# Kernel optimization log

Hardware: AMD Instinct MI355X
Metric: run time of the kernel (lower is better)

Reference implementation:

```python
import jax, jax.numpy as jnp
import numpy as np

B, P, G, NPTS = 32, 1000, 24, 72
D = 6 + NPTS
W_REG = 3.0
LENGTH = 15.0
EPS = 1e-8


def setup_inputs() -> dict:
    key = jax.random.key(0)
    k1, k2, k3 = jax.random.split(key, 3)
    preds = jax.random.uniform(k1, (B, P, D), dtype=jnp.float32)
    targets = jax.random.uniform(k2, (B, G, D), dtype=jnp.float32)
    num_gt = jax.random.randint(k3, (B,), 1, G + 1)
    masks = jnp.arange(G)[None, :] < num_gt[:, None]  # prefix validity mask, as in torch slicing
    return {"preds": preds, "targets": targets, "masks": masks, "img_w": 800, "img_h": 320}


def _assign_one(pred, target, gt_mask, img_w, img_h):
    # pred: [P, 6+n], target: [G, 6+n], gt_mask: [G] bool
    Gn = target.shape[0]
    pred = pred.at[:, 3].multiply(img_w - 1.0)
    pred = pred.at[:, 6:].multiply(img_w - 1.0)
    target = target.at[:, 3].multiply(img_w - 1.0)
    target = target.at[:, 6:].multiply(img_w - 1.0)
    ppts = pred[:, 6:]    # [P, n]
    tpts = target[:, 6:]  # [G, n]

    valid_pts = (tpts >= 0) & (tpts < img_w)                         # [G, n]
    valid_len = jnp.clip(valid_pts.sum(1).astype(pred.dtype), 1.0)
    diff = jnp.abs(ppts[:, None, :] - tpts[None, :, :]) * valid_pts[None].astype(pred.dtype)
    distances = diff.sum(-1) / valid_len[None]                       # [P, G]

    def masked_max(x):  # max over valid gts only (matches torch slice [:num_gt])
        return jnp.max(jnp.where(gt_mask[None], x, -jnp.inf))

    d_score = 1.0 - distances / (masked_max(distances) + EPS) + 0.01

    p_start = jnp.stack([pred[:, 2] * (img_h - 1.0), pred[:, 3]], axis=1)
    t_start = jnp.stack([target[:, 2] * (img_h - 1.0), target[:, 3]], axis=1)
    start_d = jnp.sqrt(jnp.sum((p_start[:, None, :] - t_start[None, :, :]) ** 2, -1))
    xy_score = 1.0 - start_d / (masked_max(start_d) + EPS) + 0.01

    theta_d = jnp.abs(pred[:, 4:5] * 180.0 - target[None, :, 4] * 180.0)  # [P, G]
    th_score = 1.0 - theta_d / (masked_max(theta_d) + EPS) + 0.01

    cls_prob = jax.nn.softmax(pred[:, :2], axis=1)[:, 1]
    cls_cost = -jnp.log(jnp.clip(cls_prob, EPS))                     # [P]

    reg_score = d_score * xy_score * th_score
    total_cost = -(reg_score ** 2) * W_REG + cls_cost[:, None]       # [P, G]

    # line_iou, unaligned (CLRNet): per-point segment overlap of length 2*LENGTH
    px1, px2 = ppts - LENGTH, ppts + LENGTH
    tx1, tx2 = tpts - LENGTH, tpts + LENGTH
    inval = (tpts < 0) | (tpts >= img_w)                             # [G, n]
    ovr = jnp.minimum(px2[:, None, :], tx2[None]) - jnp.maximum(px1[:, None, :], tx1[None])
    uni = jnp.maximum(px2[:, None, :], tx2[None]) - jnp.minimum(px1[:, None, :], tx1[None])
    ovr = jnp.where(inval[None], 0.0, ovr)
    uni = jnp.where(inval[None], 0.0, uni)
    liou = jnp.nan_to_num(ovr.sum(-1) / (uni.sum(-1) + 1e-9))        # [P, G]

    n_cand = min(4, ppts.shape[0])
    topk_ious, _ = jax.lax.top_k(liou.T, n_cand)                     # [G, k]
    dynamic_ks = jnp.clip(topk_ious.sum(1).astype(jnp.int32), 1)     # [G]

    # per-gt topk(smallest cost, k=dynamic_ks[g]) via rank < k
    ranks = jnp.argsort(jnp.argsort(total_cost, axis=0), axis=0)     # [P, G]
    matching = (ranks < dynamic_ks[None, :]) & gt_mask[None, :]      # [P, G] bool

    # conflict resolution: priors matched to >1 gts keep only the min-cost gt
    counts = matching.sum(1)
    best_g = jnp.argmin(jnp.where(gt_mask[None, :], total_cost, jnp.inf), axis=1)  # [P]
    onehot = best_g[:, None] == jnp.arange(Gn)[None, :]
    matching = jnp.where((counts > 1)[:, None], onehot, matching)

    assigned = matching.any(1)
    matched = jnp.where(assigned, jnp.argmax(matching, axis=1), -1).astype(jnp.int32)
    return assigned, matched


def reference(preds, targets, masks, img_w, img_h):
    w, h = float(img_w), float(img_h)
    fn = lambda p, t, m: _assign_one(p, t, m, w, h)
    assigned_mask, matched_targets = jax.vmap(fn)(preds, targets, masks)
    return assigned_mask, matched_targets
```

## Files before the change

kernel.cpp:

```cpp
#include <hip/hip_runtime.h>
#include <cstdint>
#include <cstddef>

#define BN 32
#define PN 1000
#define GN 24
#define NPTSN 72
#define DNN 78
#define CHN 16
#define PPC 63
#define EPSF 1e-8f
#define INF __builtin_inff()

#define OFF_DIST  0
#define OFF_LIOU  768000
#define OFF_PX    1536000
#define OFF_PY    1568000
#define OFF_PTH   1600000
#define OFF_CLS   1632000
#define OFF_PART  1664000
#define OFF_CNT   1665536
#define OFF_SELG  1697536
#define OFF_BEST  1729536

__device__ __forceinline__ unsigned ordf(float f) {
  unsigned u = __float_as_uint(f);
  return (u & 0x80000000u) ? ~u : (u | 0x80000000u);
}
__device__ __forceinline__ float unordf(unsigned u) {
  return __uint_as_float((u & 0x80000000u) ? (u ^ 0x80000000u) : ~u);
}
__device__ __forceinline__ unsigned long long shfl_xor_u64(unsigned long long v, int m) {
  int lo = __shfl_xor((int)(unsigned)v, m);
  int hi = __shfl_xor((int)(unsigned)(v >> 32), m);
  return (((unsigned long long)(unsigned)hi) << 32) | (unsigned)lo;
}

__device__ int detect_mask_layout(const void* masks, int* sflag) {
  const unsigned* mw = (const unsigned*)masks;
  if (mw[0] == 0x3f800000u) return 2;
  if (threadIdx.x == 0) *sflag = 0;
  __syncthreads();
  const unsigned char* mb = (const unsigned char*)masks;
  int local = 0;
  for (int i = threadIdx.x; i < BN * GN; i += blockDim.x)
    if ((i & 3) != 0 && mb[i] != 0) local = 1;
  if (local) atomicOr(sflag, 1);
  __syncthreads();
  return (*sflag) ? 1 : 0;
}
__device__ __forceinline__ int mask_val(const void* masks, int layout, int idx) {
  if (layout == 2) return ((const float*)masks)[idx] != 0.0f;
  if (layout == 1) return ((const unsigned char*)masks)[idx] != 0;
  return ((const int*)masks)[idx] != 0;
}

__global__ __launch_bounds__(256) void clr_k1(
    const float* __restrict__ preds, const float* __restrict__ targets,
    const void* __restrict__ masks, const int* __restrict__ imw,
    const int* __restrict__ imh, float* __restrict__ ws)
{
  const int b = blockIdx.y, c = blockIdx.x;
  const int tid = threadIdx.x;
  const int lane = tid & 63;
  const int gq = __builtin_amdgcn_readfirstlane(tid >> 6);
  const float wf = (float)imw[0];
  const float wm1 = wf - 1.0f, hm1 = (float)imh[0] - 1.0f;

  {
    int gid = (b * CHN + c) * 256 + tid;
    if (gid < BN * PN) {
      int* wsi = (int*)ws;
      wsi[OFF_CNT + gid] = 0;
      wsi[OFF_SELG + gid] = 0x7fffffff;
      ((unsigned long long*)(ws + OFF_BEST))[gid] = ~0ull;
    }
  }

  __shared__ __align__(16) float sts[GN * NPTSN];
  __shared__ __align__(16) float stw[GN * NPTSN];
  __shared__ float svl[GN], snv[GN], sgx[GN], sgy[GN], sgth[GN];
  __shared__ int sgm[GN];
  __shared__ int sng;
  __shared__ int sflag;
  __shared__ float red[4][3];

  const int mlay = detect_mask_layout(masks, &sflag);

  for (int idx = tid; idx < GN * NPTSN; idx += 256) {
    int g = idx / NPTSN, j = idx - g * NPTSN;
    float t = targets[(size_t)(b * GN + g) * DNN + 6 + j] * wm1;
    sts[idx] = t;
    stw[idx] = (t >= 0.0f && t < wf) ? 1.0f : 0.0f;
  }
  __syncthreads();
  if (tid < GN) {
    float cnt = 0.0f;
    for (int j = 0; j < NPTSN; j++) cnt += stw[tid * NPTSN + j];
    snv[tid] = cnt;
    svl[tid] = fmaxf(cnt, 1.0f);
    const float* tr = targets + (size_t)(b * GN + tid) * DNN;
    sgx[tid]  = tr[2] * hm1;
    sgy[tid]  = tr[3] * wm1;
    sgth[tid] = tr[4] * 180.0f;
    sgm[tid] = mask_val(masks, mlay, b * GN + tid);
  }
  __syncthreads();
  if (tid == 0) {
    int n = 0;
    for (int g = 0; g < GN; g++) n += sgm[g];
    sng = n;
  }
  __syncthreads();
  const int ng = sng;

  const int p = c * PPC + lane;
  const bool active = (lane < PPC) && (p < PN);
  float pp[NPTSN];
  float ppx = 0.f, ppy = 0.f, ppth = 0.f;
  if (active) {
    const float* row = preds + (size_t)(b * PN + p) * DNN;
    const float2* r2 = (const float2*)row;
    float2 c23 = r2[1], c45 = r2[2];
    ppx = c23.x * hm1; ppy = c23.y * wm1; ppth = c45.x * 180.0f;
    #pragma unroll
    for (int j = 0; j < NPTSN / 2; j++) {
      float2 v = r2[3 + j];
      pp[2 * j]     = v.x * wm1;
      pp[2 * j + 1] = v.y * wm1;
    }
    if (gq == 0) {
      float2 c01 = r2[0];
      float m = fmaxf(c01.x, c01.y);
      float e0 = expf(c01.x - m), e1 = expf(c01.y - m);
      float p1 = fmaxf(e1 / (e0 + e1), EPSF);
      ws[OFF_PX  + b * PN + p] = ppx;
      ws[OFF_PY  + b * PN + p] = ppy;
      ws[OFF_PTH + b * PN + p] = ppth;
      ws[OFF_CLS + b * PN + p] = -logf(p1);
    }
  } else {
    #pragma unroll
    for (int j = 0; j < NPTSN; j++) pp[j] = 0.0f;
  }

  float mxd = -INF, mxs = -INF, mxt = -INF;
  for (int i = 0; i < 6; i++) {
    const int g = gq + 4 * i;
    if (g >= ng) break;
    const float4* t4 = (const float4*)&sts[g * NPTSN];
    const float4* w4 = (const float4*)&stw[g * NPTSN];
    float S0 = 0.f, S1 = 0.f, S2 = 0.f, S3 = 0.f;
    #pragma unroll
    for (int jj = 0; jj < NPTSN / 4; jj++) {
      float4 t = t4[jj], w = w4[jj];
      S0 += w.x * fabsf(pp[4 * jj + 0] - t.x);
      S1 += w.y * fabsf(pp[4 * jj + 1] - t.y);
      S2 += w.z * fabsf(pp[4 * jj + 2] - t.z);
      S3 += w.w * fabsf(pp[4 * jj + 3] - t.w);
    }
    float S = (S0 + S1) + (S2 + S3);
    const float VL = svl[g], NV = snv[g];
    float dist = S / VL;
    float liou = (30.0f * NV - S) / (30.0f * NV + S + 1e-9f);
    float dx = ppx - sgx[g], dy = ppy - sgy[g];
    float sd = sqrtf(dx * dx + dy * dy);
    float td = fabsf(ppth - sgth[g]);
    if (active) {
      size_t o = (size_t)(b * GN + g) * PN + p;
      ws[OFF_DIST + o] = dist;
      ws[OFF_LIOU + o] = liou;
      mxd = fmaxf(mxd, dist);
      mxs = fmaxf(mxs, sd);
      mxt = fmaxf(mxt, td);
    }
  }

  #pragma unroll
  for (int off = 32; off; off >>= 1) {
    mxd = fmaxf(mxd, __shfl_xor(mxd, off));
    mxs = fmaxf(mxs, __shfl_xor(mxs, off));
    mxt = fmaxf(mxt, __shfl_xor(mxt, off));
  }
  if (lane == 0) { red[gq][0] = mxd; red[gq][1] = mxs; red[gq][2] = mxt; }
  __syncthreads();
  if (tid == 0) {
    float a = red[0][0], s = red[0][1], t = red[0][2];
    for (int i = 1; i < 4; i++) {
      a = fmaxf(a, red[i][0]);
      s = fmaxf(s, red[i][1]);
      t = fmaxf(t, red[i][2]);
    }
    ws[OFF_PART + (b * CHN + c) * 3 + 0] = a;
    ws[OFF_PART + (b * CHN + c) * 3 + 1] = s;
    ws[OFF_PART + (b * CHN + c) * 3 + 2] = t;
  }
}

__global__ __launch_bounds__(256) void clr_k2a(
    const float* __restrict__ targets, const void* __restrict__ masks,
    const int* __restrict__ imw, const int* __restrict__ imh,
    const float* __restrict__ cws, float* __restrict__ ws)
{
  const int g = blockIdx.x, b = blockIdx.y;
  const int bg = b * GN + g;
  __shared__ int sflag;
  const int mlay = detect_mask_layout(masks, &sflag);
  if (!mask_val(masks, mlay, bg)) return;

  const int tid = threadIdx.x;
  const int lane = tid & 63;
  const int wv = tid >> 6;
  const float hm1 = (float)imh[0] - 1.0f;
  const float wm1 = (float)imw[0] - 1.0f;

  float Md = -INF, Ms = -INF, Mt = -INF;
  for (int c2 = 0; c2 < CHN; c2++) {
    Md = fmaxf(Md, cws[OFF_PART + (b * CHN + c2) * 3 + 0]);
    Ms = fmaxf(Ms, cws[OFF_PART + (b * CHN + c2) * 3 + 1]);
    Mt = fmaxf(Mt, cws[OFF_PART + (b * CHN + c2) * 3 + 2]);
  }
  const float* tr = targets + (size_t)bg * DNN;
  const float tx = tr[2] * hm1, ty = tr[3] * wm1, tth = tr[4] * 180.0f;
  const size_t dbase = (size_t)bg * PN;
  unsigned long long* bst = (unsigned long long*)(ws + OFF_BEST);
  int* wsi = (int*)ws;

  unsigned long long ck[4], lk[4];
  #pragma unroll
  for (int i = 0; i < 4; i++) {
    int p = tid + i * 256;
    unsigned long long kc = ~0ull, kl = ~0ull;
    if (p < PN) {
      float dist = cws[OFF_DIST + dbase + p];
      float liou = cws[OFF_LIOU + dbase + p];
      float px  = cws[OFF_PX  + b * PN + p];
      float py  = cws[OFF_PY  + b * PN + p];
      float pth = cws[OFF_PTH + b * PN + p];
      float cls = cws[OFF_CLS + b * PN + p];
      float dsc = (1.0f - dist / (Md + EPSF)) + 0.01f;
      float dx = px - tx, dy = py - ty;
      float xsc = (1.0f - sqrtf(dx * dx + dy * dy) / (Ms + EPSF)) + 0.01f;
      float tsc = (1.0f - fabsf(pth - tth) / (Mt + EPSF)) + 0.01f;
      float r = (dsc * xsc) * tsc;
      float cost = -(r * r) * 3.0f + cls;
      unsigned oc = ordf(cost);
      kc = (((unsigned long long)oc) << 32) | (unsigned)p;
      kl = (((unsigned long long)(unsigned)(~ordf(liou))) << 32) | (unsigned)p;
      atomicMin(&bst[b * PN + p], (((unsigned long long)oc) << 32) | (unsigned)g);
    }
    ck[i] = kc; lk[i] = kl;
  }

  __shared__ unsigned long long ctop[4][4], ltop[4][4];
  #pragma unroll
  for (int pass = 0; pass < 4; pass++) {
    unsigned long long m = ck[0];
    #pragma unroll
    for (int i = 1; i < 4; i++) m = (ck[i] < m) ? ck[i] : m;
    #pragma unroll
    for (int off = 32; off; off >>= 1) {
      unsigned long long o = shfl_xor_u64(m, off);
      m = (o < m) ? o : m;
    }
    #pragma unroll
    for (int i = 0; i < 4; i++) if (ck[i] == m) ck[i] = ~0ull;
    if (lane == 0) ctop[wv][pass] = m;
  }
  #pragma unroll
  for (int pass = 0; pass < 4; pass++) {
    unsigned long long m = lk[0];
    #pragma unroll
    for (int i = 1; i < 4; i++) m = (lk[i] < m) ? lk[i] : m;
    #pragma unroll
    for (int off = 32; off; off >>= 1) {
      unsigned long long o = shfl_xor_u64(m, off);
      m = (o < m) ? o : m;
    }
    #pragma unroll
    for (int i = 0; i < 4; i++) if (lk[i] == m) lk[i] = ~0ull;
    if (lane == 0) ltop[wv][pass] = m;
  }
  __syncthreads();

  if (tid == 0) {
    unsigned long long c4[4] = {~0ull, ~0ull, ~0ull, ~0ull};
    unsigned long long l4[4] = {~0ull, ~0ull, ~0ull, ~0ull};
    for (int i = 0; i < 16; i++) {
      unsigned long long v = ctop[i >> 2][i & 3];
      for (int j = 0; j < 4; j++)
        if (v < c4[j]) { unsigned long long t = c4[j]; c4[j] = v; v = t; }
      v = ltop[i >> 2][i & 3];
      for (int j = 0; j < 4; j++)
        if (v < l4[j]) { unsigned long long t = l4[j]; l4[j] = v; v = t; }
    }
    float s = 0.0f;
    for (int j = 0; j < 4; j++) s += unordf(~(unsigned)(l4[j] >> 32));
    int k = (int)s;
    if (k < 1) k = 1;
    if (k > 4) k = 4;
    for (int j = 0; j < k; j++) {
      int cand = (int)(unsigned)(c4[j] & 0xffffffffu);
      atomicAdd(&wsi[OFF_CNT + b * PN + cand], 1);
      atomicMin(&wsi[OFF_SELG + b * PN + cand], g);
    }
  }
}

__global__ __launch_bounds__(256) void clr_k2b(
    const float* __restrict__ cws, int* __restrict__ out)
{
  const int i = blockIdx.x * 256 + threadIdx.x;
  if (i >= BN * PN) return;
  const int* wsi = (const int*)cws;
  const unsigned long long* bst = (const unsigned long long*)(cws + OFF_BEST);
  int cnt = wsi[OFF_CNT + i];
  int assigned = cnt > 0 ? 1 : 0;
  int matched = -1;
  if (cnt == 1) matched = wsi[OFF_SELG + i];
  else if (cnt > 1) matched = (int)(unsigned)(bst[i] & 0xffffffffull);
  out[i] = assigned;
  out[BN * PN + i] = matched;
}

extern "C" void kernel_launch(void* const* d_in, const int* in_sizes, int n_in,
                              void* d_out, int out_size, void* d_ws, size_t ws_size,
                              hipStream_t stream) {
  const float* preds   = (const float*)d_in[0];
  const float* targets = (const float*)d_in[1];
  const void*  masks   = (const void*)d_in[2];
  const int*   imw     = (const int*)d_in[3];
  const int*   imh     = (const int*)d_in[4];
  float* ws = (float*)d_ws;
  int*   out = (int*)d_out;

  hipLaunchKernelGGL(clr_k1, dim3(CHN, BN), dim3(256), 0, stream,
                     preds, targets, masks, imw, imh, ws);
  hipLaunchKernelGGL(clr_k2a, dim3(GN, BN), dim3(256), 0, stream,
                     targets, masks, imw, imh, (const float*)d_ws, ws);
  hipLaunchKernelGGL(clr_k2b, dim3((BN * PN + 255) / 256), dim3(256), 0, stream,
                     (const float*)d_ws, out);
}
```

Before: 96.21 us.

## Fuse three kernels into one cooperative kernel with grid syncs

Merges the distance, cost/top-k and finalize kernels into a single cooperative launch separated by grid-wide syncs. The per-prior atomicMin best-cost tracking is replaced by a stored cost matrix that the final phase scans. Target points are now read from global memory instead of shared-memory staging, and a fast path skips the validity test when all points are valid. The aim is to remove launch gaps and atomics, at the cost of grid-sync overhead, an extra cost-matrix write plus its INF initialization, and a dependence on all 512 blocks being co-resident.

```diff
diff --git a/kernel.cpp b/kernel.cpp
--- a/kernel.cpp
+++ b/kernel.cpp
@@ -1,6 +1,9 @@
 #include <hip/hip_runtime.h>
+#include <hip/hip_cooperative_groups.h>
 #include <cstdint>
 #include <cstddef>
+
+namespace cg = cooperative_groups;
 
 #define BN 32
 #define PN 1000
@@ -9,19 +12,20 @@
 #define DNN 78
 #define CHN 16
 #define PPC 63
+#define NBLK (CHN*BN)
 #define EPSF 1e-8f
 #define INF __builtin_inff()
 
 #define OFF_DIST  0
 #define OFF_LIOU  768000
-#define OFF_PX    1536000
-#define OFF_PY    1568000
-#define OFF_PTH   1600000
-#define OFF_CLS   1632000
-#define OFF_PART  1664000
-#define OFF_CNT   1665536
-#define OFF_SELG  1697536
-#define OFF_BEST  1729536
+#define OFF_COST  1536000
+#define OFF_PX    2304000
+#define OFF_PY    2336000
+#define OFF_PTH   2368000
+#define OFF_CLS   2400000
+#define OFF_PART  2432000
+#define OFF_CNT   2433536
+#define OFF_SELG  2465536
 
 __device__ __forceinline__ unsigned ordf(float f) {
   unsigned u = __float_as_uint(f);
@@ -55,51 +59,48 @@
   return ((const int*)masks)[idx] != 0;
 }
 
-__global__ __launch_bounds__(256) void clr_k1(
+__global__ __launch_bounds__(256, 2) void clr_fused(
     const float* __restrict__ preds, const float* __restrict__ targets,
     const void* __restrict__ masks, const int* __restrict__ imw,
-    const int* __restrict__ imh, float* __restrict__ ws)
+    const int* __restrict__ imh, float* __restrict__ ws, int* __restrict__ out)
 {
-  const int b = blockIdx.y, c = blockIdx.x;
+  const int bx = blockIdx.x;
+  const int b  = bx >> 4;
+  const int c  = bx & 15;
   const int tid = threadIdx.x;
   const int lane = tid & 63;
   const int gq = __builtin_amdgcn_readfirstlane(tid >> 6);
-  const float wf = (float)imw[0];
+  const float wf  = (float)imw[0];
   const float wm1 = wf - 1.0f, hm1 = (float)imh[0] - 1.0f;
+  int* wsi = (int*)ws;
 
   {
-    int gid = (b * CHN + c) * 256 + tid;
+    int gid = bx * 256 + tid;
     if (gid < BN * PN) {
-      int* wsi = (int*)ws;
-      wsi[OFF_CNT + gid] = 0;
+      wsi[OFF_CNT + gid]  = 0;
       wsi[OFF_SELG + gid] = 0x7fffffff;
-      ((unsigned long long*)(ws + OFF_BEST))[gid] = ~0ull;
-    }
-  }
-
-  __shared__ __align__(16) float sts[GN * NPTSN];
-  __shared__ __align__(16) float stw[GN * NPTSN];
+    }
+    for (int k = gid; k < BN * GN * PN; k += NBLK * 256)
+      ws[OFF_COST + k] = INF;
+  }
+
   __shared__ float svl[GN], snv[GN], sgx[GN], sgy[GN], sgth[GN];
   __shared__ int sgm[GN];
-  __shared__ int sng;
-  __shared__ int sflag;
+  __shared__ int sng, sflag;
   __shared__ float red[4][3];
+  __shared__ unsigned long long ctop[4][4], ltop[4][4];
 
   const int mlay = detect_mask_layout(masks, &sflag);
 
-  for (int idx = tid; idx < GN * NPTSN; idx += 256) {
-    int g = idx / NPTSN, j = idx - g * NPTSN;
-    float t = targets[(size_t)(b * GN + g) * DNN + 6 + j] * wm1;
-    sts[idx] = t;
-    stw[idx] = (t >= 0.0f && t < wf) ? 1.0f : 0.0f;
-  }
-  __syncthreads();
   if (tid < GN) {
+    const float* tr = targets + (size_t)(b * GN + tid) * DNN;
     float cnt = 0.0f;
-    for (int j = 0; j < NPTSN; j++) cnt += stw[tid * NPTSN + j];
+    for (int j = 0; j < NPTSN; j++) {
+      float ts = tr[6 + j] * wm1;
+      cnt += (ts >= 0.0f && ts < wf) ? 1.0f : 0.0f;
+    }
     snv[tid] = cnt;
     svl[tid] = fmaxf(cnt, 1.0f);
-    const float* tr = targets + (size_t)(b * GN + tid) * DNN;
     sgx[tid]  = tr[2] * hm1;
     sgy[tid]  = tr[3] * wm1;
     sgth[tid] = tr[4] * 180.0f;
@@ -112,7 +113,7 @@
     sng = n;
   }
   __syncthreads();
-  const int ng = sng;
+  const int ng = __builtin_amdgcn_readfirstlane(sng);
 
   const int p = c * PPC + lane;
   const bool active = (lane < PPC) && (p < PN);
@@ -126,8 +127,8 @@
     #pragma unroll
     for (int j = 0; j < NPTSN / 2; j++) {
       float2 v = r2[3 + j];
-      pp[2 * j]     = v.x * wm1;
-      pp[2 * j + 1] = v.y * wm1;
+      pp[2 * j]     = v.x;
+      pp[2 * j + 1] = v.y;
     }
     if (gq == 0) {
       float2 c01 = r2[0];
@@ -148,20 +149,31 @@
   for (int i = 0; i < 6; i++) {
     const int g = gq + 4 * i;
     if (g >= ng) break;
-    const float4* t4 = (const float4*)&sts[g * NPTSN];
-    const float4* w4 = (const float4*)&stw[g * NPTSN];
+    const float NV = snv[g];
+    const float* tr6 = targets + (size_t)(b * GN + g) * DNN + 6;
     float S0 = 0.f, S1 = 0.f, S2 = 0.f, S3 = 0.f;
-    #pragma unroll
-    for (int jj = 0; jj < NPTSN / 4; jj++) {
-      float4 t = t4[jj], w = w4[jj];
-      S0 += w.x * fabsf(pp[4 * jj + 0] - t.x);
-      S1 += w.y * fabsf(pp[4 * jj + 1] - t.y);
-      S2 += w.z * fabsf(pp[4 * jj + 2] - t.z);
-      S3 += w.w * fabsf(pp[4 * jj + 3] - t.w);
-    }
-    float S = (S0 + S1) + (S2 + S3);
-    const float VL = svl[g], NV = snv[g];
-    float dist = S / VL;
+    if (NV == (float)NPTSN) {
+      #pragma unroll
+      for (int jj = 0; jj < NPTSN; jj += 4) {
+        S0 += fabsf(pp[jj + 0] - tr6[jj + 0]);
+        S1 += fabsf(pp[jj + 1] - tr6[jj + 1]);
+        S2 += fabsf(pp[jj + 2] - tr6[jj + 2]);
+        S3 += fabsf(pp[jj + 3] - tr6[jj + 3]);
+      }
+    } else {
+      #pragma unroll
+      for (int jj = 0; jj < NPTSN; jj += 4) {
+        float t0 = tr6[jj + 0], t1 = tr6[jj + 1];
+        float t2 = tr6[jj + 2], t3 = tr6[jj + 3];
+        float v0 = t0 * wm1, v1 = t1 * wm1, v2 = t2 * wm1, v3 = t3 * wm1;
+        S0 += (v0 >= 0.0f && v0 < wf) ? fabsf(pp[jj + 0] - t0) : 0.0f;
+        S1 += (v1 >= 0.0f && v1 < wf) ? fabsf(pp[jj + 1] - t1) : 0.0f;
+        S2 += (v2 >= 0.0f && v2 < wf) ? fabsf(pp[jj + 2] - t2) : 0.0f;
+        S3 += (v3 >= 0.0f && v3 < wf) ? fabsf(pp[jj + 3] - t3) : 0.0f;
+      }
+    }
+    float S = ((S0 + S1) + (S2 + S3)) * wm1;
+    float dist = S / svl[g];
     float liou = (30.0f * NV - S) / (30.0f * NV + S + 1e-9f);
     float dx = ppx - sgx[g], dy = ppy - sgy[g];
     float sd = sqrtf(dx * dx + dy * dy);
@@ -191,136 +203,132 @@
       s = fmaxf(s, red[i][1]);
       t = fmaxf(t, red[i][2]);
     }
-    ws[OFF_PART + (b * CHN + c) * 3 + 0] = a;
-    ws[OFF_PART + (b * CHN + c) * 3 + 1] = s;
-    ws[OFF_PART + (b * CHN + c) * 3 + 2] = t;
-  }
-}
-
-__global__ __launch_bounds__(256) void clr_k2a(
-    const float* __restrict__ targets, const void* __restrict__ masks,
-    const int* __restrict__ imw, const int* __restrict__ imh,
-    const float* __restrict__ cws, float* __restrict__ ws)
-{
-  const int g = blockIdx.x, b = blockIdx.y;
-  const int bg = b * GN + g;
-  __shared__ int sflag;
-  const int mlay = detect_mask_layout(masks, &sflag);
-  if (!mask_val(masks, mlay, bg)) return;
-
-  const int tid = threadIdx.x;
-  const int lane = tid & 63;
-  const int wv = tid >> 6;
-  const float hm1 = (float)imh[0] - 1.0f;
-  const float wm1 = (float)imw[0] - 1.0f;
-
-  float Md = -INF, Ms = -INF, Mt = -INF;
-  for (int c2 = 0; c2 < CHN; c2++) {
-    Md = fmaxf(Md, cws[OFF_PART + (b * CHN + c2) * 3 + 0]);
-    Ms = fmaxf(Ms, cws[OFF_PART + (b * CHN + c2) * 3 + 1]);
-    Mt = fmaxf(Mt, cws[OFF_PART + (b * CHN + c2) * 3 + 2]);
-  }
-  const float* tr = targets + (size_t)bg * DNN;
-  const float tx = tr[2] * hm1, ty = tr[3] * wm1, tth = tr[4] * 180.0f;
-  const size_t dbase = (size_t)bg * PN;
-  unsigned long long* bst = (unsigned long long*)(ws + OFF_BEST);
-  int* wsi = (int*)ws;
-
-  unsigned long long ck[4], lk[4];
-  #pragma unroll
-  for (int i = 0; i < 4; i++) {
-    int p = tid + i * 256;
-    unsigned long long kc = ~0ull, kl = ~0ull;
-    if (p < PN) {
-      float dist = cws[OFF_DIST + dbase + p];
-      float liou = cws[OFF_LIOU + dbase + p];
-      float px  = cws[OFF_PX  + b * PN + p];
-      float py  = cws[OFF_PY  + b * PN + p];
-      float pth = cws[OFF_PTH + b * PN + p];
-      float cls = cws[OFF_CLS + b * PN + p];
-      float dsc = (1.0f - dist / (Md + EPSF)) + 0.01f;
-      float dx = px - tx, dy = py - ty;
-      float xsc = (1.0f - sqrtf(dx * dx + dy * dy) / (Ms + EPSF)) + 0.01f;
-      float tsc = (1.0f - fabsf(pth - tth) / (Mt + EPSF)) + 0.01f;
-      float r = (dsc * xsc) * tsc;
-      float cost = -(r * r) * 3.0f + cls;
-      unsigned oc = ordf(cost);
-      kc = (((unsigned long long)oc) << 32) | (unsigned)p;
-      kl = (((unsigned long long)(unsigned)(~ordf(liou))) << 32) | (unsigned)p;
-      atomicMin(&bst[b * PN + p], (((unsigned long long)oc) << 32) | (unsigned)g);
-    }
-    ck[i] = kc; lk[i] = kl;
-  }
-
-  __shared__ unsigned long long ctop[4][4], ltop[4][4];
-  #pragma unroll
-  for (int pass = 0; pass < 4; pass++) {
-    unsigned long long m = ck[0];
-    #pragma unroll
-    for (int i = 1; i < 4; i++) m = (ck[i] < m) ? ck[i] : m;
-    #pragma unroll
-    for (int off = 32; off; off >>= 1) {
-      unsigned long long o = shfl_xor_u64(m, off);
-      m = (o < m) ? o : m;
-    }
-    #pragma unroll
-    for (int i = 0; i < 4; i++) if (ck[i] == m) ck[i] = ~0ull;
-    if (lane == 0) ctop[wv][pass] = m;
-  }
-  #pragma unroll
-  for (int pass = 0; pass < 4; pass++) {
-    unsigned long long m = lk[0];
-    #pragma unroll
-    for (int i = 1; i < 4; i++) m = (lk[i] < m) ? lk[i] : m;
-    #pragma unroll
-    for (int off = 32; off; off >>= 1) {
-      unsigned long long o = shfl_xor_u64(m, off);
-      m = (o < m) ? o : m;
-    }
-    #pragma unroll
-    for (int i = 0; i < 4; i++) if (lk[i] == m) lk[i] = ~0ull;
-    if (lane == 0) ltop[wv][pass] = m;
-  }
-  __syncthreads();
-
-  if (tid == 0) {
-    unsigned long long c4[4] = {~0ull, ~0ull, ~0ull, ~0ull};
-    unsigned long long l4[4] = {~0ull, ~0ull, ~0ull, ~0ull};
-    for (int i = 0; i < 16; i++) {
-      unsigned long long v = ctop[i >> 2][i & 3];
-      for (int j = 0; j < 4; j++)
-        if (v < c4[j]) { unsigned long long t = c4[j]; c4[j] = v; v = t; }
-      v = ltop[i >> 2][i & 3];
-      for (int j = 0; j < 4; j++)
-        if (v < l4[j]) { unsigned long long t = l4[j]; l4[j] = v; v = t; }
-    }
-    float s = 0.0f;
-    for (int j = 0; j < 4; j++) s += unordf(~(unsigned)(l4[j] >> 32));
-    int k = (int)s;
-    if (k < 1) k = 1;
-    if (k > 4) k = 4;
-    for (int j = 0; j < k; j++) {
-      int cand = (int)(unsigned)(c4[j] & 0xffffffffu);
-      atomicAdd(&wsi[OFF_CNT + b * PN + cand], 1);
-      atomicMin(&wsi[OFF_SELG + b * PN + cand], g);
-    }
-  }
-}
-
-__global__ __launch_bounds__(256) void clr_k2b(
-    const float* __restrict__ cws, int* __restrict__ out)
-{
-  const int i = blockIdx.x * 256 + threadIdx.x;
-  if (i >= BN * PN) return;
-  const int* wsi = (const int*)cws;
-  const unsigned long long* bst = (const unsigned long long*)(cws + OFF_BEST);
-  int cnt = wsi[OFF_CNT + i];
-  int assigned = cnt > 0 ? 1 : 0;
-  int matched = -1;
-  if (cnt == 1) matched = wsi[OFF_SELG + i];
-  else if (cnt > 1) matched = (int)(unsigned)(bst[i] & 0xffffffffull);
-  out[i] = assigned;
-  out[BN * PN + i] = matched;
+    ws[OFF_PART + bx * 3 + 0] = a;
+    ws[OFF_PART + bx * 3 + 1] = s;
+    ws[OFF_PART + bx * 3 + 2] = t;
+  }
+
+  cg::this_grid().sync();
+
+  for (int task = bx; task < BN * GN; task += NBLK) {
+    const int b2 = task / GN;
+    const int g2 = task - b2 * GN;
+    if (mask_val(masks, mlay, task)) {
+      const int wv = tid >> 6;
+      float Md = -INF, Ms = -INF, Mt = -INF;
+      for (int c2 = 0; c2 < CHN; c2++) {
+        Md = fmaxf(Md, ws[OFF_PART + (b2 * CHN + c2) * 3 + 0]);
+        Ms = fmaxf(Ms, ws[OFF_PART + (b2 * CHN + c2) * 3 + 1]);
+        Mt = fmaxf(Mt, ws[OFF_PART + (b2 * CHN + c2) * 3 + 2]);
+      }
+      const float* tr = targets + (size_t)task * DNN;
+      const float tx = tr[2] * hm1, ty = tr[3] * wm1, tth = tr[4] * 180.0f;
+      const size_t dbase = (size_t)task * PN;
+
+      unsigned long long ck[4], lk[4];
+      #pragma unroll
+      for (int i = 0; i < 4; i++) {
+        int p2 = tid + i * 256;
+        unsigned long long kc = ~0ull, kl = ~0ull;
+        if (p2 < PN) {
+          float dist = ws[OFF_DIST + dbase + p2];
+          float liou = ws[OFF_LIOU + dbase + p2];
+          float px  = ws[OFF_PX  + b2 * PN + p2];
+          float py  = ws[OFF_PY  + b2 * PN + p2];
+          float pth = ws[OFF_PTH + b2 * PN + p2];
+          float cls = ws[OFF_CLS + b2 * PN + p2];
+          float dsc = (1.0f - dist / (Md + EPSF)) + 0.01f;
+          float dx = px - tx, dy = py - ty;
+          float xsc = (1.0f - sqrtf(dx * dx + dy * dy) / (Ms + EPSF)) + 0.01f;
+          float tsc = (1.0f - fabsf(pth - tth) / (Mt + EPSF)) + 0.01f;
+          float r = (dsc * xsc) * tsc;
+          float cost = -(r * r) * 3.0f + cls;
+          ws[OFF_COST + dbase + p2] = cost;
+          unsigned oc = ordf(cost);
+          kc = (((unsigned long long)oc) << 32) | (unsigned)p2;
+          kl = (((unsigned long long)(unsigned)(~ordf(liou))) << 32) | (unsigned)p2;
+        }
+        ck[i] = kc; lk[i] = kl;
+      }
+
+      #pragma unroll
+      for (int pass = 0; pass < 4; pass++) {
+        unsigned long long m = ck[0];
+        #pragma unroll
+        for (int i = 1; i < 4; i++) m = (ck[i] < m) ? ck[i] : m;
+        #pragma unroll
+        for (int off = 32; off; off >>= 1) {
+          unsigned long long o = shfl_xor_u64(m, off);
+          m = (o < m) ? o : m;
+        }
+        #pragma unroll
+        for (int i = 0; i < 4; i++) if (ck[i] == m) ck[i] = ~0ull;
+        if (lane == 0) ctop[wv][pass] = m;
+      }
+      #pragma unroll
+      for (int pass = 0; pass < 4; pass++) {
+        unsigned long long m = lk[0];
+        #pragma unroll
+        for (int i = 1; i < 4; i++) m = (lk[i] < m) ? lk[i] : m;
+        #pragma unroll
+        for (int off = 32; off; off >>= 1) {
+          unsigned long long o = shfl_xor_u64(m, off);
+          m = (o < m) ? o : m;
+        }
+        #pragma unroll
+        for (int i = 0; i < 4; i++) if (lk[i] == m) lk[i] = ~0ull;
+        if (lane == 0) ltop[wv][pass] = m;
+      }
+      __syncthreads();
+
+      if (tid == 0) {
+        unsigned long long c4[4] = {~0ull, ~0ull, ~0ull, ~0ull};
+        unsigned long long l4[4] = {~0ull, ~0ull, ~0ull, ~0ull};
+        for (int i = 0; i < 16; i++) {
+          unsigned long long v = ctop[i >> 2][i & 3];
+          for (int j = 0; j < 4; j++)
+            if (v < c4[j]) { unsigned long long t = c4[j]; c4[j] = v; v = t; }
+          v = ltop[i >> 2][i & 3];
+          for (int j = 0; j < 4; j++)
+            if (v < l4[j]) { unsigned long long t = l4[j]; l4[j] = v; v = t; }
+        }
+        float s = 0.0f;
+        for (int j = 0; j < 4; j++) s += unordf(~(unsigned)(l4[j] >> 32));
+        int k = (int)s;
+        if (k < 1) k = 1;
+        if (k > 4) k = 4;
+        for (int j = 0; j < k; j++) {
+          int cand = (int)(unsigned)(c4[j] & 0xffffffffu);
+          atomicAdd(&wsi[OFF_CNT + b2 * PN + cand], 1);
+          atomicMin(&wsi[OFF_SELG + b2 * PN + cand], g2);
+        }
+      }
+      __syncthreads();
+    }
+  }
+
+  cg::this_grid().sync();
+
+  {
+    const int i = bx * 256 + tid;
+    if (i < BN * PN) {
+      int cnt = wsi[OFF_CNT + i];
+      int matched = -1;
+      if (cnt == 1) {
+        matched = wsi[OFF_SELG + i];
+      } else if (cnt > 1) {
+        const int b3 = i / PN, p3 = i - b3 * PN;
+        float best = INF; int bgm = -1;
+        for (int g = 0; g < GN; g++) {
+          float cst = ws[OFF_COST + ((size_t)(b3 * GN + g)) * PN + p3];
+          if (cst < best) { best = cst; bgm = g; }
+        }
+        matched = bgm;
+      }
+      out[i] = (cnt > 0) ? 1 : 0;
+      out[BN * PN + i] = matched;
+    }
+  }
 }
 
 extern "C" void kernel_launch(void* const* d_in, const int* in_sizes, int n_in,
@@ -334,10 +342,8 @@
   float* ws = (float*)d_ws;
   int*   out = (int*)d_out;
 
-  hipLaunchKernelGGL(clr_k1, dim3(CHN, BN), dim3(256), 0, stream,
-                     preds, targets, masks, imw, imh, ws);
-  hipLaunchKernelGGL(clr_k2a, dim3(GN, BN), dim3(256), 0, stream,
-                     targets, masks, imw, imh, (const float*)d_ws, ws);
-  hipLaunchKernelGGL(clr_k2b, dim3((BN * PN + 255) / 256), dim3(256), 0, stream,
-                     (const float*)d_ws, out);
-}
+  void* args[7] = { (void*)&preds, (void*)&targets, (void*)&masks,
+                    (void*)&imw, (void*)&imh, (void*)&ws, (void*)&out };
+  hipLaunchCooperativeKernel((const void*)clr_fused, dim3(NBLK), dim3(256),
+                             args, 0, stream);
+}
```

New measurement: 218.8 us. 2.27x slower.

## Merge assignment and finalize kernels via cooperative grid sync, drop 64-bit atomics

Applied to the files above, without the earlier changes.

Fuses the per-gt selection kernel and the finalize kernel into one cooperative launch separated by a grid-wide sync, removing one kernel launch. Instead of a 64-bit atomicMin per prior per gt to track the min-cost gt, per-gt costs are written to a new workspace array and the finalize step scans the 24 costs only for priors matched more than once. The distance loop also gets a fast path that skips the validity weights when all points of a gt are valid. In exchange, the first kernel now writes an extra INF-initialisation of the cost array, and the grid sync requires all 768 blocks to be co-resident.

```diff
diff --git a/kernel.cpp b/kernel.cpp
--- a/kernel.cpp
+++ b/kernel.cpp
@@ -1,6 +1,9 @@
 #include <hip/hip_runtime.h>
+#include <hip/hip_cooperative_groups.h>
 #include <cstdint>
 #include <cstddef>
+
+namespace cg = cooperative_groups;
 
 #define BN 32
 #define PN 1000
@@ -14,14 +17,14 @@
 
 #define OFF_DIST  0
 #define OFF_LIOU  768000
-#define OFF_PX    1536000
-#define OFF_PY    1568000
-#define OFF_PTH   1600000
-#define OFF_CLS   1632000
-#define OFF_PART  1664000
-#define OFF_CNT   1665536
-#define OFF_SELG  1697536
-#define OFF_BEST  1729536
+#define OFF_COST  1536000
+#define OFF_PX    2304000
+#define OFF_PY    2336000
+#define OFF_PTH   2368000
+#define OFF_CLS   2400000
+#define OFF_PART  2432000
+#define OFF_CNT   2433536
+#define OFF_SELG  2465536
 
 __device__ __forceinline__ unsigned ordf(float f) {
   unsigned u = __float_as_uint(f);
@@ -69,12 +72,13 @@
 
   {
     int gid = (b * CHN + c) * 256 + tid;
+    int* wsi = (int*)ws;
     if (gid < BN * PN) {
-      int* wsi = (int*)ws;
       wsi[OFF_CNT + gid] = 0;
       wsi[OFF_SELG + gid] = 0x7fffffff;
-      ((unsigned long long*)(ws + OFF_BEST))[gid] = ~0ull;
-    }
+    }
+    for (int k = gid; k < BN * GN * PN; k += CHN * BN * 256)
+      ws[OFF_COST + k] = INF;
   }
 
   __shared__ __align__(16) float sts[GN * NPTSN];
@@ -148,19 +152,31 @@
   for (int i = 0; i < 6; i++) {
     const int g = gq + 4 * i;
     if (g >= ng) break;
+    const float NV = snv[g];
     const float4* t4 = (const float4*)&sts[g * NPTSN];
-    const float4* w4 = (const float4*)&stw[g * NPTSN];
     float S0 = 0.f, S1 = 0.f, S2 = 0.f, S3 = 0.f;
-    #pragma unroll
-    for (int jj = 0; jj < NPTSN / 4; jj++) {
-      float4 t = t4[jj], w = w4[jj];
-      S0 += w.x * fabsf(pp[4 * jj + 0] - t.x);
-      S1 += w.y * fabsf(pp[4 * jj + 1] - t.y);
-      S2 += w.z * fabsf(pp[4 * jj + 2] - t.z);
-      S3 += w.w * fabsf(pp[4 * jj + 3] - t.w);
+    if (NV == (float)NPTSN) {
+      #pragma unroll
+      for (int jj = 0; jj < NPTSN / 4; jj++) {
+        float4 t = t4[jj];
+        S0 += fabsf(pp[4 * jj + 0] - t.x);
+        S1 += fabsf(pp[4 * jj + 1] - t.y);
+        S2 += fabsf(pp[4 * jj + 2] - t.z);
+        S3 += fabsf(pp[4 * jj + 3] - t.w);
+      }
+    } else {
+      const float4* w4 = (const float4*)&stw[g * NPTSN];
+      #pragma unroll
+      for (int jj = 0; jj < NPTSN / 4; jj++) {
+        float4 t = t4[jj], w = w4[jj];
+        S0 += w.x * fabsf(pp[4 * jj + 0] - t.x);
+        S1 += w.y * fabsf(pp[4 * jj + 1] - t.y);
+        S2 += w.z * fabsf(pp[4 * jj + 2] - t.z);
+        S3 += w.w * fabsf(pp[4 * jj + 3] - t.w);
+      }
     }
     float S = (S0 + S1) + (S2 + S3);
-    const float VL = svl[g], NV = snv[g];
+    const float VL = svl[g];
     float dist = S / VL;
     float liou = (30.0f * NV - S) / (30.0f * NV + S + 1e-9f);
     float dx = ppx - sgx[g], dy = ppy - sgy[g];
@@ -197,130 +213,138 @@
   }
 }
 
-__global__ __launch_bounds__(256) void clr_k2a(
+__global__ __launch_bounds__(256, 3) void clr_k2(
     const float* __restrict__ targets, const void* __restrict__ masks,
     const int* __restrict__ imw, const int* __restrict__ imh,
-    const float* __restrict__ cws, float* __restrict__ ws)
+    float* __restrict__ ws, int* __restrict__ out)
 {
   const int g = blockIdx.x, b = blockIdx.y;
   const int bg = b * GN + g;
-  __shared__ int sflag;
-  const int mlay = detect_mask_layout(masks, &sflag);
-  if (!mask_val(masks, mlay, bg)) return;
-
   const int tid = threadIdx.x;
   const int lane = tid & 63;
   const int wv = tid >> 6;
-  const float hm1 = (float)imh[0] - 1.0f;
-  const float wm1 = (float)imw[0] - 1.0f;
-
-  float Md = -INF, Ms = -INF, Mt = -INF;
-  for (int c2 = 0; c2 < CHN; c2++) {
-    Md = fmaxf(Md, cws[OFF_PART + (b * CHN + c2) * 3 + 0]);
-    Ms = fmaxf(Ms, cws[OFF_PART + (b * CHN + c2) * 3 + 1]);
-    Mt = fmaxf(Mt, cws[OFF_PART + (b * CHN + c2) * 3 + 2]);
-  }
-  const float* tr = targets + (size_t)bg * DNN;
-  const float tx = tr[2] * hm1, ty = tr[3] * wm1, tth = tr[4] * 180.0f;
-  const size_t dbase = (size_t)bg * PN;
-  unsigned long long* bst = (unsigned long long*)(ws + OFF_BEST);
   int* wsi = (int*)ws;
 
-  unsigned long long ck[4], lk[4];
-  #pragma unroll
-  for (int i = 0; i < 4; i++) {
-    int p = tid + i * 256;
-    unsigned long long kc = ~0ull, kl = ~0ull;
-    if (p < PN) {
-      float dist = cws[OFF_DIST + dbase + p];
-      float liou = cws[OFF_LIOU + dbase + p];
-      float px  = cws[OFF_PX  + b * PN + p];
-      float py  = cws[OFF_PY  + b * PN + p];
-      float pth = cws[OFF_PTH + b * PN + p];
-      float cls = cws[OFF_CLS + b * PN + p];
-      float dsc = (1.0f - dist / (Md + EPSF)) + 0.01f;
-      float dx = px - tx, dy = py - ty;
-      float xsc = (1.0f - sqrtf(dx * dx + dy * dy) / (Ms + EPSF)) + 0.01f;
-      float tsc = (1.0f - fabsf(pth - tth) / (Mt + EPSF)) + 0.01f;
-      float r = (dsc * xsc) * tsc;
-      float cost = -(r * r) * 3.0f + cls;
-      unsigned oc = ordf(cost);
-      kc = (((unsigned long long)oc) << 32) | (unsigned)p;
-      kl = (((unsigned long long)(unsigned)(~ordf(liou))) << 32) | (unsigned)p;
-      atomicMin(&bst[b * PN + p], (((unsigned long long)oc) << 32) | (unsigned)g);
-    }
-    ck[i] = kc; lk[i] = kl;
-  }
-
+  __shared__ int sflag;
   __shared__ unsigned long long ctop[4][4], ltop[4][4];
-  #pragma unroll
-  for (int pass = 0; pass < 4; pass++) {
-    unsigned long long m = ck[0];
-    #pragma unroll
-    for (int i = 1; i < 4; i++) m = (ck[i] < m) ? ck[i] : m;
-    #pragma unroll
-    for (int off = 32; off; off >>= 1) {
-      unsigned long long o = shfl_xor_u64(m, off);
-      m = (o < m) ? o : m;
-    }
-    #pragma unroll
-    for (int i = 0; i < 4; i++) if (ck[i] == m) ck[i] = ~0ull;
-    if (lane == 0) ctop[wv][pass] = m;
-  }
-  #pragma unroll
-  for (int pass = 0; pass < 4; pass++) {
-    unsigned long long m = lk[0];
-    #pragma unroll
-    for (int i = 1; i < 4; i++) m = (lk[i] < m) ? lk[i] : m;
-    #pragma unroll
-    for (int off = 32; off; off >>= 1) {
-      unsigned long long o = shfl_xor_u64(m, off);
-      m = (o < m) ? o : m;
-    }
-    #pragma unroll
-    for (int i = 0; i < 4; i++) if (lk[i] == m) lk[i] = ~0ull;
-    if (lane == 0) ltop[wv][pass] = m;
-  }
-  __syncthreads();
-
-  if (tid == 0) {
-    unsigned long long c4[4] = {~0ull, ~0ull, ~0ull, ~0ull};
-    unsigned long long l4[4] = {~0ull, ~0ull, ~0ull, ~0ull};
-    for (int i = 0; i < 16; i++) {
-      unsigned long long v = ctop[i >> 2][i & 3];
-      for (int j = 0; j < 4; j++)
-        if (v < c4[j]) { unsigned long long t = c4[j]; c4[j] = v; v = t; }
-      v = ltop[i >> 2][i & 3];
-      for (int j = 0; j < 4; j++)
-        if (v < l4[j]) { unsigned long long t = l4[j]; l4[j] = v; v = t; }
-    }
-    float s = 0.0f;
-    for (int j = 0; j < 4; j++) s += unordf(~(unsigned)(l4[j] >> 32));
-    int k = (int)s;
-    if (k < 1) k = 1;
-    if (k > 4) k = 4;
-    for (int j = 0; j < k; j++) {
-      int cand = (int)(unsigned)(c4[j] & 0xffffffffu);
-      atomicAdd(&wsi[OFF_CNT + b * PN + cand], 1);
-      atomicMin(&wsi[OFF_SELG + b * PN + cand], g);
-    }
-  }
-}
-
-__global__ __launch_bounds__(256) void clr_k2b(
-    const float* __restrict__ cws, int* __restrict__ out)
-{
-  const int i = blockIdx.x * 256 + threadIdx.x;
-  if (i >= BN * PN) return;
-  const int* wsi = (const int*)cws;
-  const unsigned long long* bst = (const unsigned long long*)(cws + OFF_BEST);
-  int cnt = wsi[OFF_CNT + i];
-  int assigned = cnt > 0 ? 1 : 0;
-  int matched = -1;
-  if (cnt == 1) matched = wsi[OFF_SELG + i];
-  else if (cnt > 1) matched = (int)(unsigned)(bst[i] & 0xffffffffull);
-  out[i] = assigned;
-  out[BN * PN + i] = matched;
+  const int mlay = detect_mask_layout(masks, &sflag);
+
+  if (mask_val(masks, mlay, bg)) {
+    const float hm1 = (float)imh[0] - 1.0f;
+    const float wm1 = (float)imw[0] - 1.0f;
+
+    float Md = -INF, Ms = -INF, Mt = -INF;
+    for (int c2 = 0; c2 < CHN; c2++) {
+      Md = fmaxf(Md, ws[OFF_PART + (b * CHN + c2) * 3 + 0]);
+      Ms = fmaxf(Ms, ws[OFF_PART + (b * CHN + c2) * 3 + 1]);
+      Mt = fmaxf(Mt, ws[OFF_PART + (b * CHN + c2) * 3 + 2]);
+    }
+    const float* tr = targets + (size_t)bg * DNN;
+    const float tx = tr[2] * hm1, ty = tr[3] * wm1, tth = tr[4] * 180.0f;
+    const size_t dbase = (size_t)bg * PN;
+
+    unsigned long long ck[4], lk[4];
+    #pragma unroll
+    for (int i = 0; i < 4; i++) {
+      int p = tid + i * 256;
+      unsigned long long kc = ~0ull, kl = ~0ull;
+      if (p < PN) {
+        float dist = ws[OFF_DIST + dbase + p];
+        float liou = ws[OFF_LIOU + dbase + p];
+        float px  = ws[OFF_PX  + b * PN + p];
+        float py  = ws[OFF_PY  + b * PN + p];
+        float pth = ws[OFF_PTH + b * PN + p];
+        float cls = ws[OFF_CLS + b * PN + p];
+        float dsc = (1.0f - dist / (Md + EPSF)) + 0.01f;
+        float dx = px - tx, dy = py - ty;
+        float xsc = (1.0f - sqrtf(dx * dx + dy * dy) / (Ms + EPSF)) + 0.01f;
+        float tsc = (1.0f - fabsf(pth - tth) / (Mt + EPSF)) + 0.01f;
+        float r = (dsc * xsc) * tsc;
+        float cost = -(r * r) * 3.0f + cls;
+        ws[OFF_COST + dbase + p] = cost;
+        unsigned oc = ordf(cost);
+        kc = (((unsigned long long)oc) << 32) | (unsigned)p;
+        kl = (((unsigned long long)(unsigned)(~ordf(liou))) << 32) | (unsigned)p;
+      }
+      ck[i] = kc; lk[i] = kl;
+    }
+
+    #pragma unroll
+    for (int pass = 0; pass < 4; pass++) {
+      unsigned long long m = ck[0];
+      #pragma unroll
+      for (int i = 1; i < 4; i++) m = (ck[i] < m) ? ck[i] : m;
+      #pragma unroll
+      for (int off = 32; off; off >>= 1) {
+        unsigned long long o = shfl_xor_u64(m, off);
+        m = (o < m) ? o : m;
+      }
+      #pragma unroll
+      for (int i = 0; i < 4; i++) if (ck[i] == m) ck[i] = ~0ull;
+      if (lane == 0) ctop[wv][pass] = m;
+    }
+    #pragma unroll
+    for (int pass = 0; pass < 4; pass++) {
+      unsigned long long m = lk[0];
+      #pragma unroll
+      for (int i = 1; i < 4; i++) m = (lk[i] < m) ? lk[i] : m;
+      #pragma unroll
+      for (int off = 32; off; off >>= 1) {
+        unsigned long long o = shfl_xor_u64(m, off);
+        m = (o < m) ? o : m;
+      }
+      #pragma unroll
+      for (int i = 0; i < 4; i++) if (lk[i] == m) lk[i] = ~0ull;
+      if (lane == 0) ltop[wv][pass] = m;
+    }
+    __syncthreads();
+
+    if (tid == 0) {
+      unsigned long long c4[4] = {~0ull, ~0ull, ~0ull, ~0ull};
+      unsigned long long l4[4] = {~0ull, ~0ull, ~0ull, ~0ull};
+      for (int i = 0; i < 16; i++) {
+        unsigned long long v = ctop[i >> 2][i & 3];
+        for (int j = 0; j < 4; j++)
+          if (v < c4[j]) { unsigned long long t = c4[j]; c4[j] = v; v = t; }
+        v = ltop[i >> 2][i & 3];
+        for (int j = 0; j < 4; j++)
+          if (v < l4[j]) { unsigned long long t = l4[j]; l4[j] = v; v = t; }
+      }
+      float s = 0.0f;
+      for (int j = 0; j < 4; j++) s += unordf(~(unsigned)(l4[j] >> 32));
+      int k = (int)s;
+      if (k < 1) k = 1;
+      if (k > 4) k = 4;
+      for (int j = 0; j < k; j++) {
+        int cand = (int)(unsigned)(c4[j] & 0xffffffffu);
+        atomicAdd(&wsi[OFF_CNT + b * PN + cand], 1);
+        atomicMin(&wsi[OFF_SELG + b * PN + cand], g);
+      }
+    }
+  }
+
+  cg::this_grid().sync();
+
+  {
+    const int i = bg * 256 + tid;
+    if (i < BN * PN) {
+      int cnt = wsi[OFF_CNT + i];
+      int matched = -1;
+      if (cnt == 1) {
+        matched = wsi[OFF_SELG + i];
+      } else if (cnt > 1) {
+        const int b3 = i / PN, p3 = i - b3 * PN;
+        float best = INF; int bgm = -1;
+        for (int gg = 0; gg < GN; gg++) {
+          float cst = ws[OFF_COST + ((size_t)(b3 * GN + gg)) * PN + p3];
+          if (cst < best) { best = cst; bgm = gg; }
+        }
+        matched = bgm;
+      }
+      out[i] = (cnt > 0) ? 1 : 0;
+      out[BN * PN + i] = matched;
+    }
+  }
 }
 
 extern "C" void kernel_launch(void* const* d_in, const int* in_sizes, int n_in,
@@ -336,8 +360,9 @@
 
   hipLaunchKernelGGL(clr_k1, dim3(CHN, BN), dim3(256), 0, stream,
                      preds, targets, masks, imw, imh, ws);
-  hipLaunchKernelGGL(clr_k2a, dim3(GN, BN), dim3(256), 0, stream,
-                     targets, masks, imw, imh, (const float*)d_ws, ws);
-  hipLaunchKernelGGL(clr_k2b, dim3((BN * PN + 255) / 256), dim3(256), 0, stream,
-                     (const float*)d_ws, out);
-}
+
+  void* args[6] = { (void*)&targets, (void*)&masks, (void*)&imw,
+                    (void*)&imh, (void*)&ws, (void*)&out };
+  hipLaunchCooperativeKernel((const void*)clr_k2, dim3(GN, BN), dim3(256),
+                             args, 0, stream);
+}
```

New measurement: 176.9 us. +83.9%, slower.
